# Kernel tuning notes

Hardware: AMD Instinct MI355X
Metric: run time of the kernel (lower is better)

## Reference

```python
import jax, jax.numpy as jnp
import numpy as np
from jax import lax

NL = 4        # n_layers
V = 32000     # vocab_size
D = 768       # embedding_dim (d_model)
L = 2048      # seq_len
B = 1         # batch
E = 1536      # d_inner = expand * d_model
N = 8         # d_state
R = 48        # dt_rank = ceil(768/16)
K = 3         # d_conv


def rmsnorm(x, w, eps=1e-6):
    return x * w * lax.rsqrt(jnp.mean(x * x, axis=-1, keepdims=True) + eps)


def causal_dwconv(x, w, b):
    # depthwise causal conv1d; x: (B,L,E), w: (K,E), b: (E,)
    xp = jnp.pad(x, ((0, 0), (K - 1, 0), (0, 0)))
    y = sum(xp[:, k:k + x.shape[1], :] * w[k] for k in range(K))
    return y + b


def selective_scan(dt, A, Bm, C, u):
    # dt,u: (B,L,E); A: (E,N); Bm,C: (B,L,N)
    dA = jnp.exp(dt[..., None] * A)                      # (B,L,E,N)
    dBu = dt[..., None] * Bm[:, :, None, :] * u[..., None]  # (B,L,E,N)

    def step(h, xs):
        a, bu, c = xs
        h = a * h + bu                                   # (B,E,N)
        return h, jnp.einsum('ben,bn->be', h, c)

    h0 = jnp.zeros((u.shape[0], E, N), u.dtype)
    _, ys = lax.scan(step, h0, (dA.swapaxes(0, 1), dBu.swapaxes(0, 1), C.swapaxes(0, 1)))
    return ys.swapaxes(0, 1)                             # (B,L,E)


def mamba_block(x, Wi, bi, cw, cb, Wx, Wdt, bdt, Alog, Dsk, Wo, bo):
    xz = x @ Wi + bi                                     # (B,L,2E)
    u, res = jnp.split(xz, 2, axis=-1)
    u = jax.nn.silu(causal_dwconv(u, cw, cb))
    dbl = u @ Wx                                         # (B,L,R+2N)
    dt, Bm, C = dbl[..., :R], dbl[..., R:R + N], dbl[..., R + N:]
    dt = jax.nn.softplus(dt @ Wdt + bdt)                 # (B,L,E)
    A = -jnp.exp(Alog)                                   # (E,N)
    y = selective_scan(dt, A, Bm, C, u) + u * Dsk
    y = y * jax.nn.silu(res)
    return y @ Wo + bo


def setup_inputs() -> dict:
    key = jax.random.key(0)
    ks = jax.random.split(key, 10)
    s = 0.02
    return {
        'inputs': jax.random.randint(ks[0], (B, L), 0, V),
        'emb': jax.random.normal(ks[1], (V, D), jnp.float32) * s,
        'W_in': jax.random.normal(ks[2], (NL, D, 2 * E), jnp.float32) * s,
        'b_in': jnp.zeros((NL, 2 * E), jnp.float32),
        'conv_w': jax.random.normal(ks[3], (NL, K, E), jnp.float32) * s,
        'conv_b': jnp.zeros((NL, E), jnp.float32),
        'W_x': jax.random.normal(ks[4], (NL, E, R + 2 * N), jnp.float32) * s,
        'W_dt': jax.random.normal(ks[5], (NL, R, E), jnp.float32) * s,
        'b_dt': jax.random.normal(ks[6], (NL, E), jnp.float32) * s,
        'A_log': jnp.tile(jnp.log(jnp.arange(1, N + 1, dtype=jnp.float32)), (NL, E, 1)),
        'D_skip': jnp.ones((NL, E), jnp.float32),
        'W_out': jax.random.normal(ks[7], (NL, E, D), jnp.float32) * s,
        'b_out': jnp.zeros((NL, D), jnp.float32),
        'norm_w': jnp.ones((NL, D), jnp.float32),
        'normf_w': jnp.ones((D,), jnp.float32),
        'W_lm': jax.random.normal(ks[8], (D, V), jnp.float32) * s,
    }


def reference(inputs, emb, W_in, b_in, conv_w, conv_b, W_x, W_dt, b_dt, A_log, D_skip, W_out, b_out, norm_w, normf_w, W_lm):
    x = emb[inputs]                                      # (B,L,D)
    for i in range(NL):
        x = x + mamba_block(rmsnorm(x, norm_w[i]), W_in[i], b_in[i], conv_w[i], conv_b[i],
                            W_x[i], W_dt[i], b_dt[i], A_log[i], D_skip[i], W_out[i], b_out[i])
    x = rmsnorm(x, normf_w)
    return x @ W_lm                                      # logits (B,L,V)
```

## Files before the change

kernel.cpp:

```cpp
#include <hip/hip_runtime.h>
#include <hip/hip_bf16.h>
#include <cstdint>
#include <cstddef>

#define L_SEQ 2048
#define DIM   768
#define EDIM  1536
#define NLAY  4
#define NST   8
#define RNK   48
#define VOC   32000
#define NCH   64
#define CHS   32
#define TT    16

typedef __bf16 bf16x8 __attribute__((ext_vector_type(8)));
typedef float  f32x4  __attribute__((ext_vector_type(4)));

typedef __attribute__((address_space(3))) void lds_void;
typedef const __attribute__((address_space(1))) void gbl_void;

__device__ __forceinline__ void gld_lds16(const void* g, void* l) {
    __builtin_amdgcn_global_load_lds((gbl_void*)g, (lds_void*)l, 16, 0, 0);
}

__device__ __forceinline__ float bf2f(__hip_bfloat16 v) { return __bfloat162float(v); }

__global__ __launch_bounds__(256)
void prep_k(const float* __restrict__ W_in, const float* __restrict__ W_out,
            const float* __restrict__ W_lm, const float* __restrict__ W_x,
            __hip_bfloat16* __restrict__ WiT, __hip_bfloat16* __restrict__ WoT,
            __hip_bfloat16* __restrict__ WlmT, __hip_bfloat16* __restrict__ WxT)
{
    __shared__ float tile[32][33];
    int bid = blockIdx.x;
    const float* src; __hip_bfloat16* dst;
    int R, C, c0, r0;
    if (bid < 9216) {
        const int lz = bid / 2304, rem = bid % 2304;
        R = 768; C = 3072; c0 = (rem % 96) * 32; r0 = (rem / 96) * 32;
        src = W_in + (size_t)lz * 768 * 3072; dst = WiT + (size_t)lz * 3072 * 768;
    } else if (bid < 9216 + 4608) {
        bid -= 9216;
        const int lz = bid / 1152, rem = bid % 1152;
        R = 1536; C = 768; c0 = (rem % 24) * 32; r0 = (rem / 24) * 32;
        src = W_out + (size_t)lz * 1536 * 768; dst = WoT + (size_t)lz * 768 * 1536;
    } else if (bid < 9216 + 4608 + 24000) {
        bid -= 9216 + 4608;
        R = 768; C = 32000; c0 = (bid % 1000) * 32; r0 = (bid / 1000) * 32;
        src = W_lm; dst = WlmT;
    } else {
        bid -= 9216 + 4608 + 24000;
        const int lz = bid / 96, rem = bid % 96;
        R = 1536; C = 64; c0 = (rem % 2) * 32; r0 = (rem / 2) * 32;
        src = W_x + (size_t)lz * 1536 * 64; dst = WxT + (size_t)lz * 64 * 1536;
    }
    const int tx = threadIdx.x & 31;
    const int ty = threadIdx.x >> 5;
#pragma unroll
    for (int j = 0; j < 32; j += 8)
        tile[ty + j][tx] = src[(size_t)(r0 + ty + j) * C + c0 + tx];
    __syncthreads();
#pragma unroll
    for (int j = 0; j < 32; j += 8)
        dst[(size_t)(c0 + ty + j) * R + r0 + tx] = __float2bfloat16(tile[tx][ty + j]);
}

template<bool EMB>
__global__ __launch_bounds__(256)
void rmsnorm4_k(const float* __restrict__ src, const float* __restrict__ w,
                __hip_bfloat16* __restrict__ out,
                const int* __restrict__ ids, const float* __restrict__ emb,
                float* __restrict__ xcopy)
{
    const int row  = blockIdx.x * 4 + (threadIdx.x >> 6);
    const int lane = threadIdx.x & 63;
    const float* xr;
    if constexpr (EMB) xr = emb + (size_t)ids[row] * DIM;
    else               xr = src + (size_t)row * DIM;
    float v[12];
    float s = 0.f;
#pragma unroll
    for (int j = 0; j < 12; ++j) { v[j] = xr[lane + j * 64]; s += v[j] * v[j]; }
#pragma unroll
    for (int m = 32; m >= 1; m >>= 1) s += __shfl_xor(s, m, 64);
    const float sc = rsqrtf(s * (1.0f / DIM) + 1e-6f);
    __hip_bfloat16* o = out + (size_t)row * DIM;
#pragma unroll
    for (int j = 0; j < 12; ++j)
        o[lane + j * 64] = __float2bfloat16(v[j] * w[lane + j * 64] * sc);
    if constexpr (EMB) {
        float* xc = xcopy + (size_t)row * DIM;
#pragma unroll
        for (int j = 0; j < 12; ++j) xc[lane + j * 64] = v[j];
    }
}

template<int EPI, int BM, int BN, int BK, typename OT>
__global__ __launch_bounds__(256)
void gemm_bf16(const __hip_bfloat16* __restrict__ A,
               const __hip_bfloat16* __restrict__ BT,
               const float* __restrict__ bias,
               OT* __restrict__ C,
               int M, int N, int K)
{
    constexpr int WM = BM / 2, WN = BN / 2;
    constexpr int MF = WM / 16, NF = WN / 16;
    constexpr int AOPS = BM * BK * 2 / 4096;
    constexpr int BOPS = BN * BK * 2 / 4096;
    static_assert(AOPS + BOPS == 4, "vmcnt literal assumes 4 ops/stage");

    __shared__ __hip_bfloat16 As[2][BM * BK];
    __shared__ __hip_bfloat16 Bs[2][BN * BK];

    const int tid  = threadIdx.x;
    const int lane = tid & 63, wid = tid >> 6;
    const int wr = wid >> 1, wc = wid & 1;

    const int nwg = gridDim.x;
    int wg = blockIdx.x;
    if ((nwg & 7) == 0) wg = (wg & 7) * (nwg >> 3) + (wg >> 3);
    const int mblks = M / BM;
    const int m0 = (wg % mblks) * BM;
    const int n0 = (wg / mblks) * BN;

    f32x4 acc[MF][NF] = {};

    auto stage = [&](int b, int k0) {
#pragma unroll
        for (int i = 0; i < AOPS; ++i) {
            int row, colE;
            if constexpr (BK == 32) { row = i * 64 + (tid >> 2); colE = (((tid & 3) ^ ((tid >> 3) & 3)) << 3); }
            else                    { row = i * 32 + (tid >> 3); colE = (((tid & 7) ^ ((tid >> 3) & 7)) << 3); }
            gld_lds16(A + (size_t)(m0 + row) * K + k0 + colE,
                      (char*)As[b] + i * 4096 + wid * 1024);
        }
#pragma unroll
        for (int i = 0; i < BOPS; ++i) {
            int row, colE;
            if constexpr (BK == 32) { row = i * 64 + (tid >> 2); colE = (((tid & 3) ^ ((tid >> 3) & 3)) << 3); }
            else                    { row = i * 32 + (tid >> 3); colE = (((tid & 7) ^ ((tid >> 3) & 7)) << 3); }
            gld_lds16(BT + (size_t)(n0 + row) * K + k0 + colE,
                      (char*)Bs[b] + i * 4096 + wid * 1024);
        }
    };

    const int NT = K / BK;
    stage(0, 0);

    const int rr   = lane & 15;
    const int kq16 = (lane >> 4) << 4;

    for (int kt = 0; kt < NT; ++kt) {
        const int cur = kt & 1;
        if (kt + 1 < NT) {
            stage(cur ^ 1, (kt + 1) * BK);
            asm volatile("s_waitcnt vmcnt(4)" ::: "memory");
        } else {
            asm volatile("s_waitcnt vmcnt(0)" ::: "memory");
        }
        __syncthreads();

        const char* AsB = (const char*)As[cur];
        const char* BsB = (const char*)Bs[cur];
#pragma unroll
        for (int ks = 0; ks < BK / 32; ++ks) {
            bf16x8 af[MF], bfr[NF];
#pragma unroll
            for (int m = 0; m < MF; ++m) {
                const int row = wr * WM + m * 16 + rr;
                const int swz = (BK == 32) ? (((row >> 1) & 3) << 4) : ((row & 7) << 4);
                af[m] = *(const bf16x8*)(AsB + ((row * (BK * 2) + ks * 64 + kq16) ^ swz));
            }
#pragma unroll
            for (int n = 0; n < NF; ++n) {
                const int row = wc * WN + n * 16 + rr;
                const int swz = (BK == 32) ? (((row >> 1) & 3) << 4) : ((row & 7) << 4);
                bfr[n] = *(const bf16x8*)(BsB + ((row * (BK * 2) + ks * 64 + kq16) ^ swz));
            }
#pragma unroll
            for (int m = 0; m < MF; ++m)
#pragma unroll
                for (int n = 0; n < NF; ++n)
                    acc[m][n] = __builtin_amdgcn_mfma_f32_16x16x32_bf16(af[m], bfr[n], acc[m][n], 0, 0, 0);
        }
        __syncthreads();
    }

    const int row0 = m0 + wr * WM + ((lane >> 4) * 4);
    const int col0 = n0 + wc * WN + (lane & 15);
#pragma unroll
    for (int m = 0; m < MF; ++m)
#pragma unroll
        for (int n = 0; n < NF; ++n) {
            const int c = col0 + n * 16;
#pragma unroll
            for (int j = 0; j < 4; ++j) {
                const int r = row0 + m * 16 + j;
                const float v = acc[m][n][j];
                const size_t o = (size_t)r * N + c;
                if constexpr (EPI == 0) {
                    const float z = v + bias[c];
                    if constexpr (__is_same(OT, float)) C[o] = z;
                    else                                C[o] = __float2bfloat16(z);
                } else {
                    C[o] += v + bias[c];
                }
            }
        }
}

__global__ __launch_bounds__(512, 2)
void gemm8_bf16(const __hip_bfloat16* __restrict__ A,
                const __hip_bfloat16* __restrict__ BT,
                float* __restrict__ C,
                int M, int N, int K)
{
    __shared__ uint4 lds_u4[8192];
    char* Aring = (char*)lds_u4;
    char* Bring = (char*)lds_u4 + 65536;

    const int tid  = threadIdx.x;
    const int lane = tid & 63, wid = tid >> 6;
    const int wr = wid >> 2, wc = wid & 3;

    const int nwg = gridDim.x;
    int wg = blockIdx.x;
    if ((nwg & 7) == 0) wg = (wg & 7) * (nwg >> 3) + (wg >> 3);
    const int mblks = M >> 8;
    const int m0 = (wg % mblks) * 256;
    const int n0 = (wg / mblks) * 256;
    const int NT = K >> 6;

    const int rA   = wid * 8 + (lane >> 3);
    const int colE = (((lane & 7) ^ ((lane >> 3) & 7)) << 3);
    const int ldsb = wid * 1024;

    const int rr   = lane & 15;
    const int kq16 = (lane >> 4) << 4;
    const int rbB  = (wc & 1) * 64;

    f32x4 acc[8][4] = {};
    bf16x8 areg[4][2], breg[4][2];

#define STAGE8(SRC, BASE0, TL, TC, H, RING)                                           \
    {                                                                                 \
        const int _slot = ((2 * (TL) + (H)) & 3);                                     \
        const __hip_bfloat16* _g = (SRC) + (size_t)((BASE0) + (H) * 128 + rA) * K     \
                                        + (size_t)(TC) * 64 + colE;                   \
        char* _l = (RING) + _slot * 16384 + ldsb;                                     \
        gld_lds16(_g, _l);                                                            \
        gld_lds16(_g + (size_t)64 * K, _l + 8192);                                    \
    }

#define READ_A8(MH)                                                                   \
    _Pragma("unroll")                                                                 \
    for (int _m = 0; _m < 4; ++_m) {                                                  \
        _Pragma("unroll")                                                             \
        for (int _ks = 0; _ks < 2; ++_ks) {                                           \
            const int _rh = (MH) * 64 + _m * 16 + rr;                                 \
            const int _by = (_rh * 128 + _ks * 64 + kq16) ^ ((_rh & 7) << 4);         \
            areg[_m][_ks] = *(const bf16x8*)(sAp + _by);                              \
        }                                                                             \
    }

#define READ_B8(NH)                                                                   \
    _Pragma("unroll")                                                                 \
    for (int _n = 0; _n < 2; ++_n) {                                                  \
        _Pragma("unroll")                                                             \
        for (int _ks = 0; _ks < 2; ++_ks) {                                           \
            const int _rh = rbB + (NH) * 32 + _n * 16 + rr;                           \
            const int _by = (_rh * 128 + _ks * 64 + kq16) ^ ((_rh & 7) << 4);         \
            breg[(NH) * 2 + _n][_ks] = *(const bf16x8*)(sBp + _by);                   \
        }                                                                             \
    }

#define MFMA_QUAD8(MH, NH)                                                            \
    __builtin_amdgcn_s_setprio(1);                                                    \
    _Pragma("unroll")                                                                 \
    for (int _ks = 0; _ks < 2; ++_ks)                                                 \
        _Pragma("unroll")                                                             \
        for (int _m = 0; _m < 4; ++_m)                                                \
            _Pragma("unroll")                                                         \
            for (int _n = 0; _n < 2; ++_n)                                            \
                acc[(MH) * 4 + _m][(NH) * 2 + _n] =                                   \
                    __builtin_amdgcn_mfma_f32_16x16x32_bf16(                          \
                        areg[_m][_ks], breg[(NH) * 2 + _n][_ks],                      \
                        acc[(MH) * 4 + _m][(NH) * 2 + _n], 0, 0, 0);                  \
    __builtin_amdgcn_s_setprio(0);

    STAGE8(A,  m0, 0, 0, 0, Aring);
    STAGE8(A,  m0, 0, 0, 1, Aring);
    STAGE8(BT, n0, 0, 0, 0, Bring);
    STAGE8(BT, n0, 0, 0, 1, Bring);
    {
        const int t1p = (NT > 1) ? 1 : 0;
        STAGE8(BT, n0, 1, t1p, 0, Bring);
        STAGE8(BT, n0, 1, t1p, 1, Bring);
    }
    asm volatile("s_waitcnt vmcnt(4)" ::: "memory");
    __builtin_amdgcn_s_barrier();

    for (int kt = 0; kt < NT; ++kt) {
        const char* sAp = Aring + (((2 * kt + wr) & 3) << 14);
        const char* sBp = Bring + (((2 * kt + (wc >> 1)) & 3) << 14);
        const int tn1 = (kt + 1 < NT) ? kt + 1 : NT - 1;
        const int tn2 = (kt + 2 < NT) ? kt + 2 : NT - 1;

        READ_A8(0)
        READ_B8(0)
        STAGE8(A, m0, kt + 1, tn1, 0, Aring);
        __builtin_amdgcn_s_barrier();
        MFMA_QUAD8(0, 0)
        __builtin_amdgcn_s_barrier();

        READ_B8(1)
        STAGE8(A, m0, kt + 1, tn1, 1, Aring);
        __builtin_amdgcn_s_barrier();
        MFMA_QUAD8(0, 1)
        __builtin_amdgcn_s_barrier();

        READ_A8(1)
        STAGE8(BT, n0, kt + 2, tn2, 0, Bring);
        __builtin_amdgcn_s_barrier();
        MFMA_QUAD8(1, 0)
        __builtin_amdgcn_s_barrier();

        STAGE8(BT, n0, kt + 2, tn2, 1, Bring);
        __builtin_amdgcn_s_barrier();
        MFMA_QUAD8(1, 1)
        asm volatile("s_waitcnt vmcnt(4)" ::: "memory");
        __builtin_amdgcn_s_barrier();
    }

    const int row0 = m0 + wr * 128 + ((lane >> 4) * 4);
    const int col0 = n0 + wc * 64 + (lane & 15);
#pragma unroll
    for (int m = 0; m < 8; ++m)
#pragma unroll
        for (int n = 0; n < 4; ++n) {
            const int c = col0 + n * 16;
#pragma unroll
            for (int j = 0; j < 4; ++j)
                C[(size_t)(row0 + m * 16 + j) * N + c] = acc[m][n][j];
        }
#undef STAGE8
#undef READ_A8
#undef READ_B8
#undef MFMA_QUAD8
}

__global__ __launch_bounds__(256)
void mid_k(const __hip_bfloat16* __restrict__ xz, const float* __restrict__ cw,
           const float* __restrict__ cb, const __hip_bfloat16* __restrict__ WxT,
           const float* __restrict__ Wdt, const float* __restrict__ bdt,
           __hip_bfloat16* __restrict__ u_f, float* __restrict__ dbl,
           float* __restrict__ dtb)
{
    __shared__ __hip_bfloat16 us[TT][EDIM + 8];
    __shared__ float dbs[TT][64];
    const int tid = threadIdx.x;
    const int t0  = blockIdx.x * TT;

#pragma unroll
    for (int j = 0; j < EDIM / 256; ++j) {
        const int e = tid + j * 256;
        const float w0 = cw[e], w1 = cw[EDIM + e], w2 = cw[2 * EDIM + e], b = cb[e];
        float xm2 = (t0 >= 2) ? bf2f(xz[(size_t)(t0 - 2) * (2 * EDIM) + e]) : 0.f;
        float xm1 = (t0 >= 1) ? bf2f(xz[(size_t)(t0 - 1) * (2 * EDIM) + e]) : 0.f;
#pragma unroll
        for (int tt = 0; tt < TT; ++tt) {
            const float xc = bf2f(xz[(size_t)(t0 + tt) * (2 * EDIM) + e]);
            float a = b + w0 * xm2 + w1 * xm1 + w2 * xc;
            a = a / (1.f + __expf(-a));
            const __hip_bfloat16 ab = __float2bfloat16(a);
            us[tt][e] = ab;
            u_f[(size_t)(t0 + tt) * EDIM + e] = ab;
            xm2 = xm1; xm1 = xc;
        }
    }
    __syncthreads();

    {
        const int w = tid >> 6, lane = tid & 63;
        const int rr = lane & 15, kq = (lane >> 4) * 8;
        f32x4 acc = {};
        const __hip_bfloat16* bw = WxT + (size_t)(w * 16 + rr) * EDIM;
#pragma unroll 4
        for (int k0 = 0; k0 < EDIM; k0 += 32) {
            const bf16x8 af  = *(const bf16x8*)(&us[rr][k0 + kq]);
            const bf16x8 bfr = *(const bf16x8*)(bw + k0 + kq);
            acc = __builtin_amdgcn_mfma_f32_16x16x32_bf16(af, bfr, acc, 0, 0, 0);
        }
        const int nn = w * 16 + (lane & 15);
#pragma unroll
        for (int j = 0; j < 4; ++j) {
            const int tt2 = (lane >> 4) * 4 + j;
            dbs[tt2][nn] = acc[j];
            dbl[(size_t)(t0 + tt2) * 64 + nn] = acc[j];
        }
    }
    __syncthreads();

#pragma unroll 1
    for (int j = 0; j < EDIM / 256; ++j) {
        const int e = tid + j * 256;
        float wreg[RNK];
#pragma unroll
        for (int r = 0; r < RNK; ++r) wreg[r] = Wdt[(size_t)r * EDIM + e];
        const float b = bdt[e];
#pragma unroll 1
        for (int tt = 0; tt < TT; ++tt) {
            float acc = b;
#pragma unroll
            for (int r = 0; r < RNK; ++r) acc += dbs[tt][r] * wreg[r];
            const float ax = fabsf(acc);
            dtb[(size_t)(t0 + tt) * EDIM + e] = fmaxf(acc, 0.f) + log1pf(__expf(-ax));
        }
    }
}

__global__ __launch_bounds__(64)
void scanA_k(const float* __restrict__ dt, const __hip_bfloat16* __restrict__ u_f,
             const float* __restrict__ dbl, const float* __restrict__ alog,
             float* __restrict__ Pb, float* __restrict__ Hb)
{
    const int lane = threadIdx.x;
    const int e  = blockIdx.x * 64 + lane;
    const int c  = blockIdx.y;
    const int t0 = c * CHS;
    __shared__ float BC[CHS][16];
    if (lane < CHS) {
        const float4* s4 = (const float4*)(dbl + (size_t)(t0 + lane) * 64 + 48);
        float4* d4 = (float4*)(&BC[lane][0]);
        d4[0] = s4[0]; d4[1] = s4[1]; d4[2] = s4[2]; d4[3] = s4[3];
    }
    __syncthreads();
    float A8[NST], h[NST], P[NST];
#pragma unroll
    for (int n = 0; n < NST; ++n) {
        A8[n] = -__expf(alog[(size_t)e * NST + n]);
        h[n] = 0.f; P[n] = 1.f;
    }
    float pdt[8], pu[8];
#pragma unroll
    for (int j = 0; j < 8; ++j) {
        pdt[j] = dt [(size_t)(t0 + j) * EDIM + e];
        pu [j] = bf2f(u_f[(size_t)(t0 + j) * EDIM + e]);
    }
    for (int tb = 0; tb < CHS; tb += 8) {
        float cdt[8], cu[8];
#pragma unroll
        for (int j = 0; j < 8; ++j) { cdt[j] = pdt[j]; cu[j] = pu[j]; }
        if (tb + 8 < CHS) {
#pragma unroll
            for (int j = 0; j < 8; ++j) {
                pdt[j] = dt [(size_t)(t0 + tb + 8 + j) * EDIM + e];
                pu [j] = bf2f(u_f[(size_t)(t0 + tb + 8 + j) * EDIM + e]);
            }
        }
#pragma unroll
        for (int j = 0; j < 8; ++j) {
            const float du = cdt[j] * cu[j];
#pragma unroll
            for (int n = 0; n < NST; ++n) {
                const float dA = __expf(cdt[j] * A8[n]);
                h[n] = dA * h[n] + du * BC[tb + j][n];
                P[n] *= dA;
            }
        }
    }
    const size_t o = ((size_t)c * EDIM + e) * NST;
#pragma unroll
    for (int n = 0; n < NST; ++n) { Pb[o + n] = P[n]; Hb[o + n] = h[n]; }
}

__global__ __launch_bounds__(64)
void scanC_k(const float* __restrict__ dt, const __hip_bfloat16* __restrict__ u_f,
             const float* __restrict__ dbl, const float* __restrict__ alog,
             const float* __restrict__ Pb, const float* __restrict__ Hb,
             const float* __restrict__ Dsk,
             const __hip_bfloat16* __restrict__ xz, __hip_bfloat16* __restrict__ ybf)
{
    const int lane = threadIdx.x;
    const int e  = blockIdx.x * 64 + lane;
    const int c  = blockIdx.y;
    const int t0 = c * CHS;
    __shared__ float BC[CHS][16];
    if (lane < CHS) {
        const float4* s4 = (const float4*)(dbl + (size_t)(t0 + lane) * 64 + 48);
        float4* d4 = (float4*)(&BC[lane][0]);
        d4[0] = s4[0]; d4[1] = s4[1]; d4[2] = s4[2]; d4[3] = s4[3];
    }
    __syncthreads();
    float A8[NST], h[NST];
#pragma unroll
    for (int n = 0; n < NST; ++n) {
        A8[n] = -__expf(alog[(size_t)e * NST + n]);
        h[n]  = 0.f;
    }
    for (int cc = 0; cc < c; ++cc) {
        const size_t o = ((size_t)cc * EDIM + e) * NST;
        const float4 p0 = *(const float4*)(Pb + o);
        const float4 p1 = *(const float4*)(Pb + o + 4);
        const float4 q0 = *(const float4*)(Hb + o);
        const float4 q1 = *(const float4*)(Hb + o + 4);
        h[0] = p0.x * h[0] + q0.x;  h[1] = p0.y * h[1] + q0.y;
        h[2] = p0.z * h[2] + q0.z;  h[3] = p0.w * h[3] + q0.w;
        h[4] = p1.x * h[4] + q1.x;  h[5] = p1.y * h[5] + q1.y;
        h[6] = p1.z * h[6] + q1.z;  h[7] = p1.w * h[7] + q1.w;
    }
    const float Dv = Dsk[e];
    float pdt[8], pu[8], pr[8];
#pragma unroll
    for (int j = 0; j < 8; ++j) {
        pdt[j] = dt [(size_t)(t0 + j) * EDIM + e];
        pu [j] = bf2f(u_f[(size_t)(t0 + j) * EDIM + e]);
        pr [j] = bf2f(xz [(size_t)(t0 + j) * (2 * EDIM) + EDIM + e]);
    }
    for (int tb = 0; tb < CHS; tb += 8) {
        float cdt[8], cu[8], cr[8];
#pragma unroll
        for (int j = 0; j < 8; ++j) { cdt[j] = pdt[j]; cu[j] = pu[j]; cr[j] = pr[j]; }
        if (tb + 8 < CHS) {
#pragma unroll
            for (int j = 0; j < 8; ++j) {
                pdt[j] = dt [(size_t)(t0 + tb + 8 + j) * EDIM + e];
                pu [j] = bf2f(u_f[(size_t)(t0 + tb + 8 + j) * EDIM + e]);
                pr [j] = bf2f(xz [(size_t)(t0 + tb + 8 + j) * (2 * EDIM) + EDIM + e]);
            }
        }
#pragma unroll
        for (int j = 0; j < 8; ++j) {
            const float du = cdt[j] * cu[j];
            float y = 0.f;
#pragma unroll
            for (int n = 0; n < NST; ++n) {
                const float dA = __expf(cdt[j] * A8[n]);
                h[n] = dA * h[n] + du * BC[tb + j][n];
                y += h[n] * BC[tb + j][8 + n];
            }
            y += cu[j] * Dv;
            y *= cr[j] / (1.f + __expf(-cr[j]));
            ybf[(size_t)(t0 + tb + j) * EDIM + e] = __float2bfloat16(y);
        }
    }
}

extern "C" void kernel_launch(void* const* d_in, const int* in_sizes, int n_in,
                              void* d_out, int out_size, void* d_ws, size_t ws_size,
                              hipStream_t stream)
{
    const int*   ids     = (const int*)  d_in[0];
    const float* emb     = (const float*)d_in[1];
    const float* W_in    = (const float*)d_in[2];
    const float* b_in    = (const float*)d_in[3];
    const float* conv_w  = (const float*)d_in[4];
    const float* conv_b  = (const float*)d_in[5];
    const float* W_x     = (const float*)d_in[6];
    const float* W_dt    = (const float*)d_in[7];
    const float* b_dt    = (const float*)d_in[8];
    const float* A_log   = (const float*)d_in[9];
    const float* D_skip  = (const float*)d_in[10];
    const float* W_out   = (const float*)d_in[11];
    const float* b_out   = (const float*)d_in[12];
    const float* norm_w  = (const float*)d_in[13];
    const float* normf_w = (const float*)d_in[14];
    const float* W_lm    = (const float*)d_in[15];
    float* out = (float*)d_out;
    (void)in_sizes; (void)n_in; (void)out_size; (void)ws_size;

    char* ws = (char*)d_ws;
    size_t off = 0;
    auto alloc = [&](size_t b) -> void* {
        void* p = ws + off;
        off += (b + 255) & ~(size_t)255;
        return p;
    };
    __hip_bfloat16* WiT  = (__hip_bfloat16*)alloc((size_t)NLAY * 3072 * 768 * 2);
    __hip_bfloat16* WoT  = (__hip_bfloat16*)alloc((size_t)NLAY * 768 * 1536 * 2);
    __hip_bfloat16* WlmT = (__hip_bfloat16*)alloc((size_t)VOC * 768 * 2);
    __hip_bfloat16* WxT  = (__hip_bfloat16*)alloc((size_t)NLAY * 64 * EDIM * 2);
    float* x    = (float*)alloc((size_t)L_SEQ * DIM * 4);
    __hip_bfloat16* xn  = (__hip_bfloat16*)alloc((size_t)L_SEQ * DIM * 2);
    __hip_bfloat16* xz  = (__hip_bfloat16*)alloc((size_t)L_SEQ * 2 * EDIM * 2);
    __hip_bfloat16* u_f = (__hip_bfloat16*)alloc((size_t)L_SEQ * EDIM * 2);
    float* dblb = (float*)alloc((size_t)L_SEQ * 64 * 4);
    float* dtb  = (float*)alloc((size_t)L_SEQ * EDIM * 4);
    __hip_bfloat16* ybf = (__hip_bfloat16*)alloc((size_t)L_SEQ * EDIM * 2);
    float* Pb   = (float*)alloc((size_t)NCH * EDIM * NST * 4);
    float* Hb   = (float*)alloc((size_t)NCH * EDIM * NST * 4);

    prep_k<<<dim3(9216 + 4608 + 24000 + 384), 256, 0, stream>>>(
        W_in, W_out, W_lm, W_x, WiT, WoT, WlmT, WxT);

    rmsnorm4_k<true><<<dim3(L_SEQ / 4), 256, 0, stream>>>(
        nullptr, norm_w, xn, ids, emb, x);

    for (int l = 0; l < NLAY; ++l) {
        if (l > 0)
            rmsnorm4_k<false><<<dim3(L_SEQ / 4), 256, 0, stream>>>(
                x, norm_w + l * DIM, xn, nullptr, nullptr, nullptr);
        gemm_bf16<0, 128, 128, 32, __hip_bfloat16>
            <<<dim3((L_SEQ / 128) * (3072 / 128)), 256, 0, stream>>>(
            xn, WiT + (size_t)l * 3072 * 768, b_in + l * 2 * EDIM, xz, L_SEQ, 2 * EDIM, DIM);
        mid_k<<<dim3(L_SEQ / TT), 256, 0, stream>>>(
            xz, conv_w + l * 3 * EDIM, conv_b + l * EDIM,
            WxT + (size_t)l * 64 * EDIM,
            W_dt + (size_t)l * RNK * EDIM, b_dt + l * EDIM,
            u_f, dblb, dtb);
        scanA_k<<<dim3(EDIM / 64, NCH), 64, 0, stream>>>(
            dtb, u_f, dblb, A_log + (size_t)l * EDIM * NST, Pb, Hb);
        scanC_k<<<dim3(EDIM / 64, NCH), 64, 0, stream>>>(
            dtb, u_f, dblb, A_log + (size_t)l * EDIM * NST, Pb, Hb,
            D_skip + l * EDIM, xz, ybf);
        gemm_bf16<1, 64, 64, 64, float>
            <<<dim3((L_SEQ / 64) * (768 / 64)), 256, 0, stream>>>(
            ybf, WoT + (size_t)l * 768 * 1536, b_out + l * DIM, x, L_SEQ, DIM, EDIM);
    }

    rmsnorm4_k<false><<<dim3(L_SEQ / 4), 256, 0, stream>>>(
        x, normf_w, xn, nullptr, nullptr, nullptr);
    gemm8_bf16<<<dim3((VOC / 256) * (L_SEQ / 256)), 512, 0, stream>>>(
        xn, WlmT, out, L_SEQ, VOC, DIM);
}
```

Baseline: 788.3 us.

## Add separate inter-chunk scan kernel, halve chunk size, and retile in-proj GEMM

Adds a scanB kernel that runs the sequential carry over chunk states once per (e,n) and writes each chunk's incoming state, so scanC no longer re-walks every earlier chunk. That quadratic per-block prefix work is what it targets. Chunk size drops from 32 to 16 and the chunk count doubles, giving the scan kernels more parallel blocks. The in-projection GEMM tile changes from 128x128 to 128x64 for more workgroups, with the vmcnt wait generalized to 3 ops per stage; this costs an extra launch plus a Hin buffer round trip.

```diff
diff --git a/kernel.cpp b/kernel.cpp
--- a/kernel.cpp
+++ b/kernel.cpp
@@ -10,8 +10,8 @@
 #define NST   8
 #define RNK   48
 #define VOC   32000
-#define NCH   64
-#define CHS   32
+#define NCH   128
+#define CHS   16
 #define TT    16
 
 typedef __bf16 bf16x8 __attribute__((ext_vector_type(8)));
@@ -108,7 +108,8 @@
     constexpr int MF = WM / 16, NF = WN / 16;
     constexpr int AOPS = BM * BK * 2 / 4096;
     constexpr int BOPS = BN * BK * 2 / 4096;
-    static_assert(AOPS + BOPS == 4, "vmcnt literal assumes 4 ops/stage");
+    constexpr int SOPS = AOPS + BOPS;
+    static_assert(SOPS == 3 || SOPS == 4, "vmcnt literal");
 
     __shared__ __hip_bfloat16 As[2][BM * BK];
     __shared__ __hip_bfloat16 Bs[2][BN * BK];
@@ -155,7 +156,10 @@
         const int cur = kt & 1;
         if (kt + 1 < NT) {
             stage(cur ^ 1, (kt + 1) * BK);
-            asm volatile("s_waitcnt vmcnt(4)" ::: "memory");
+            if constexpr (SOPS == 3)
+                asm volatile("s_waitcnt vmcnt(3)" ::: "memory");
+            else
+                asm volatile("s_waitcnt vmcnt(4)" ::: "memory");
         } else {
             asm volatile("s_waitcnt vmcnt(0)" ::: "memory");
         }
@@ -475,11 +479,24 @@
     for (int n = 0; n < NST; ++n) { Pb[o + n] = P[n]; Hb[o + n] = h[n]; }
 }
 
+__global__ __launch_bounds__(256)
+void scanB_k(const float* __restrict__ Pb, const float* __restrict__ Hb,
+             float* __restrict__ Hin)
+{
+    const int idx = blockIdx.x * 256 + threadIdx.x;
+    float h = 0.f;
+#pragma unroll 8
+    for (int c = 0; c < NCH; ++c) {
+        const size_t o = (size_t)c * EDIM * NST + idx;
+        Hin[o] = h;
+        h = Pb[o] * h + Hb[o];
+    }
+}
+
 __global__ __launch_bounds__(64)
 void scanC_k(const float* __restrict__ dt, const __hip_bfloat16* __restrict__ u_f,
              const float* __restrict__ dbl, const float* __restrict__ alog,
-             const float* __restrict__ Pb, const float* __restrict__ Hb,
-             const float* __restrict__ Dsk,
+             const float* __restrict__ Hin, const float* __restrict__ Dsk,
              const __hip_bfloat16* __restrict__ xz, __hip_bfloat16* __restrict__ ybf)
 {
     const int lane = threadIdx.x;
@@ -497,18 +514,7 @@
 #pragma unroll
     for (int n = 0; n < NST; ++n) {
         A8[n] = -__expf(alog[(size_t)e * NST + n]);
-        h[n]  = 0.f;
-    }
-    for (int cc = 0; cc < c; ++cc) {
-        const size_t o = ((size_t)cc * EDIM + e) * NST;
-        const float4 p0 = *(const float4*)(Pb + o);
-        const float4 p1 = *(const float4*)(Pb + o + 4);
-        const float4 q0 = *(const float4*)(Hb + o);
-        const float4 q1 = *(const float4*)(Hb + o + 4);
-        h[0] = p0.x * h[0] + q0.x;  h[1] = p0.y * h[1] + q0.y;
-        h[2] = p0.z * h[2] + q0.z;  h[3] = p0.w * h[3] + q0.w;
-        h[4] = p1.x * h[4] + q1.x;  h[5] = p1.y * h[5] + q1.y;
-        h[6] = p1.z * h[6] + q1.z;  h[7] = p1.w * h[7] + q1.w;
+        h[n]  = Hin[(size_t)c * EDIM * NST + (size_t)e * NST + n];
     }
     const float Dv = Dsk[e];
     float pdt[8], pu[8], pr[8];
@@ -590,6 +596,7 @@
     __hip_bfloat16* ybf = (__hip_bfloat16*)alloc((size_t)L_SEQ * EDIM * 2);
     float* Pb   = (float*)alloc((size_t)NCH * EDIM * NST * 4);
     float* Hb   = (float*)alloc((size_t)NCH * EDIM * NST * 4);
+    float* Hin  = (float*)alloc((size_t)NCH * EDIM * NST * 4);
 
     prep_k<<<dim3(9216 + 4608 + 24000 + 384), 256, 0, stream>>>(
         W_in, W_out, W_lm, W_x, WiT, WoT, WlmT, WxT);
@@ -601,8 +608,8 @@
         if (l > 0)
             rmsnorm4_k<false><<<dim3(L_SEQ / 4), 256, 0, stream>>>(
                 x, norm_w + l * DIM, xn, nullptr, nullptr, nullptr);
-        gemm_bf16<0, 128, 128, 32, __hip_bfloat16>
-            <<<dim3((L_SEQ / 128) * (3072 / 128)), 256, 0, stream>>>(
+        gemm_bf16<0, 128, 64, 32, __hip_bfloat16>
+            <<<dim3((L_SEQ / 128) * (3072 / 64)), 256, 0, stream>>>(
             xn, WiT + (size_t)l * 3072 * 768, b_in + l * 2 * EDIM, xz, L_SEQ, 2 * EDIM, DIM);
         mid_k<<<dim3(L_SEQ / TT), 256, 0, stream>>>(
             xz, conv_w + l * 3 * EDIM, conv_b + l * EDIM,
@@ -611,9 +618,9 @@
             u_f, dblb, dtb);
         scanA_k<<<dim3(EDIM / 64, NCH), 64, 0, stream>>>(
             dtb, u_f, dblb, A_log + (size_t)l * EDIM * NST, Pb, Hb);
+        scanB_k<<<dim3(EDIM * NST / 256), 256, 0, stream>>>(Pb, Hb, Hin);
         scanC_k<<<dim3(EDIM / 64, NCH), 64, 0, stream>>>(
-            dtb, u_f, dblb, A_log + (size_t)l * EDIM * NST, Pb, Hb,
-            D_skip + l * EDIM, xz, ybf);
+            dtb, u_f, dblb, A_log + (size_t)l * EDIM * NST, Hin, D_skip + l * EDIM, xz, ybf);
         gemm_bf16<1, 64, 64, 64, float>
             <<<dim3((L_SEQ / 64) * (768 / 64)), 256, 0, stream>>>(
             ybf, WoT + (size_t)l * 768 * 1536, b_out + l * DIM, x, L_SEQ, DIM, EDIM);
```

Result: no change. 779.5 us (-1.1%).
